# Optimization experiments

Measured on AMD Instinct MI355X. Metric: run time of the kernel, lower is better.

The kernel has to match this reference:

```python
import jax, jax.numpy as jnp
import numpy as np

N_NODES = 20000
NEG_SLOPE = 0.2  # PyG GATConv default leaky_relu slope


def segment_softmax(e, dst, num_segments):
    # e: [E, H] edge logits, softmax over edges sharing the same dst node
    m = jax.ops.segment_max(e, dst, num_segments=num_segments)
    ex = jnp.exp(e - m[dst])
    s = jax.ops.segment_sum(ex, dst, num_segments=num_segments)
    return ex / (s[dst] + 1e-16)


def gat_conv(x, src, dst, W, att_src, att_dst, bias, concat):
    # PyG GATConv (add_self_loops handled by caller). W: [Fin, H*C], att_*: [H, C]
    N = x.shape[0]
    H, C = att_src.shape
    h = (x @ W).reshape(N, H, C)
    a_src = jnp.einsum('nhc,hc->nh', h, att_src)  # [N, H]
    a_dst = jnp.einsum('nhc,hc->nh', h, att_dst)
    e = jax.nn.leaky_relu(a_src[src] + a_dst[dst], NEG_SLOPE)  # [E, H]
    alpha = segment_softmax(e, dst, N)
    msg = alpha[:, :, None] * h[src]  # [E, H, C]
    out = jax.ops.segment_sum(msg, dst, num_segments=N)  # [N, H, C]
    out = out.reshape(N, H * C) if concat else out.mean(axis=1)
    return out + bias


def add_self_loops(edge_index, num_nodes):
    loops = jnp.arange(num_nodes, dtype=edge_index.dtype)
    src = jnp.concatenate([edge_index[0], loops])
    dst = jnp.concatenate([edge_index[1], loops])
    return src, dst


def setup_inputs() -> dict:
    key = jax.random.key(0)
    ks = jax.random.split(key, 24)
    Fin, Hd, Hh, C2, Md = 1280, 256, 4, 128, 1024

    def w(k, shape, fan_in):
        return (jax.random.normal(k, shape, jnp.float32) * (1.0 / np.sqrt(fan_in))).astype(jnp.float32)

    return {
        'x': jax.random.normal(ks[0], (N_NODES, Fin), jnp.float32),
        'edge_index': jax.random.randint(ks[1], (2, 200000), 0, N_NODES, jnp.int32),
        'mutation_idx': 12345,
        'mutation_site_diff': jax.random.normal(ks[2], (1, Md), jnp.float32),
        # mutation_diff_processor: 1024 -> 128 -> 128
        'W_mut1': w(ks[3], (Md, 128), Md), 'b_mut1': jnp.zeros((128,), jnp.float32),
        'W_mut2': w(ks[4], (128, 128), 128), 'b_mut2': jnp.zeros((128,), jnp.float32),
        # GATConv1: Fin -> 256, 4 heads, concat
        'gat1_W': w(ks[5], (Fin, Hh * Hd), Fin),
        'gat1_as': w(ks[6], (Hh, Hd), Hd), 'gat1_ad': w(ks[7], (Hh, Hd), Hd),
        'gat1_b': jnp.zeros((Hh * Hd,), jnp.float32),
        # GATConv2: 1024 -> 128, 1 head
        'gat2_W': w(ks[8], (Hh * Hd, C2), Hh * Hd),
        'gat2_as': w(ks[9], (1, C2), C2), 'gat2_ad': w(ks[10], (1, C2), C2),
        'gat2_b': jnp.zeros((C2,), jnp.float32),
        # binding_predictor: 256 -> 128 -> 32 -> 1
        'W_p1': w(ks[11], (C2 + 128, 128), C2 + 128), 'b_p1': jnp.zeros((128,), jnp.float32),
        'W_p2': w(ks[12], (128, 32), 128), 'b_p2': jnp.zeros((32,), jnp.float32),
        'W_p3': w(ks[13], (32, 1), 32), 'b_p3': jnp.zeros((1,), jnp.float32),
    }


def reference(x, edge_index, mutation_idx, mutation_site_diff,
              W_mut1, b_mut1, W_mut2, b_mut2,
              gat1_W, gat1_as, gat1_ad, gat1_b,
              gat2_W, gat2_as, gat2_ad, gat2_b,
              W_p1, b_p1, W_p2, b_p2, W_p3, b_p3):
    src, dst = add_self_loops(edge_index, x.shape[0])
    # mutation diff MLP (dropout = identity at eval)
    pmd = jax.nn.relu(mutation_site_diff @ W_mut1 + b_mut1) @ W_mut2 + b_mut2
    h = jax.nn.relu(gat_conv(x, src, dst, gat1_W, gat1_as, gat1_ad, gat1_b, concat=True))
    h = jax.nn.relu(gat_conv(h, src, dst, gat2_W, gat2_as, gat2_ad, gat2_b, concat=False))
    feat = h[mutation_idx:mutation_idx + 1]  # [1, 128]
    z = jnp.concatenate([feat, pmd], axis=-1)
    z = jax.nn.relu(z @ W_p1 + b_p1)
    z = jax.nn.relu(z @ W_p2 + b_p2)
    return z @ W_p3 + b_p3
```

## Files before the change

### kernel.cpp

```cpp
#include <hip/hip_runtime.h>
#include <hip/hip_bf16.h>

#define NNODES 20000
#define NE_RAW 200000
#define NE_TOT 220000
#define MAX1   128
#define MAX2   512
#define MAXE1  4096
#define MAXE2  256
#define FIN    1280
#define FH     1024
#define HC     256
#define NHEAD  4
#define C2     128
#define CAPE   512
#define KCK    64
#define NKC    20
#define HH_GEMM_BLOCKS 320

__device__ __forceinline__ float lrelu(float x){ return x >= 0.f ? x : 0.2f * x; }

__global__ void k_init(int* cnt, int* slot1, int* slot2){
  int i = blockIdx.x * 256 + threadIdx.x;
  if (i < NNODES){ slot1[i] = -1; slot2[i] = -1; }
  if (i < 8) cnt[i] = 0;
}

__global__ void k_scan1(const int* __restrict__ ei, const int* __restrict__ mip,
                        int* cnt, int* slot1, int* S1, int* E2){
  int e = blockIdx.x * 256 + threadIdx.x;
  if (e >= NE_TOT) return;
  int mi = mip[0];
  int src, dst;
  if (e < NE_RAW){ src = ei[e]; dst = ei[NE_RAW + e]; }
  else { src = e - NE_RAW; dst = src; }
  if (dst != mi) return;
  int p = atomicAdd(&cnt[3], 1);
  if (p < MAXE2) E2[p] = src;
  if (atomicCAS(&slot1[src], -1, -9) == -1){
    int idx = atomicAdd(&cnt[0], 1);
    if (idx < MAX1){ S1[idx] = src; slot1[src] = idx; }
  }
}

__global__ void k_scan2(const int* __restrict__ ei, int* cnt,
                        const int* __restrict__ slot1, int* slot2,
                        int* S2, int* E1s, int* E1d){
  int e = blockIdx.x * 256 + threadIdx.x;
  if (e >= NE_TOT) return;
  int src, dst;
  if (e < NE_RAW){ src = ei[e]; dst = ei[NE_RAW + e]; }
  else { src = e - NE_RAW; dst = src; }
  if (slot1[dst] < 0) return;
  int p = atomicAdd(&cnt[2], 1);
  if (p < MAXE1){ E1s[p] = src; E1d[p] = dst; }
  if (atomicCAS(&slot2[src], -1, -9) == -1){
    int idx = atomicAdd(&cnt[1], 1);
    if (idx < MAX2){ S2[idx] = src; slot2[src] = idx; }
  }
}

__global__ __launch_bounds__(256) void k_hh(
    const float* __restrict__ x, const float* __restrict__ W1,
    const float* __restrict__ msd, const float* __restrict__ Wm1,
    const float* __restrict__ bm1,
    const int* __restrict__ cnt, const int* __restrict__ S2,
    float* __restrict__ hpart, float* __restrict__ r1){
  int t = threadIdx.x;
  if (blockIdx.x >= HH_GEMM_BLOCKS){
    __shared__ float red[256];
    int b   = blockIdx.x - HH_GEMM_BLOCKS;
    int col = b * 32 + (t & 31);
    int sl  = t >> 5;
    float s = 0.f;
    for (int k = sl * 128; k < sl * 128 + 128; ++k)
      s += msd[k] * Wm1[k * C2 + col];
    red[t] = s;
    __syncthreads();
    if (t < 32){
      float v = 0.f;
      #pragma unroll
      for (int q = 0; q < 8; ++q) v += red[q * 32 + t];
      v += bm1[col];
      r1[col] = v > 0.f ? v : 0.f;
    }
    return;
  }
  __shared__ float Wl[KCK][128];
  __shared__ float Xl[KCK][32];
  int bid = blockIdx.x;
  int rs = bid & 1, ct = (bid >> 1) & 7, kc = bid >> 4;
  int k0 = kc * KCK, c0 = ct * 128;
  int n2 = cnt[1]; if (n2 > MAX2) n2 = MAX2;
  for (int idx = t; idx < 2048; idx += 256){
    int r = idx >> 5, c4 = idx & 31;
    *(float4*)&Wl[r][c4 * 4] = *(const float4*)(W1 + (long)(k0 + r) * FH + c0 + c4 * 4);
  }
  int nRG = (n2 + 31) >> 5;
  int cth = t & 31, rth = t >> 5;
  for (int rg = rs; rg < nRG; rg += 2){
    int r0 = rg * 32;
    __syncthreads();
    for (int idx = t; idx < 512; idx += 256){
      int r = idx & 31, kq = idx >> 5;
      float4 v = make_float4(0.f, 0.f, 0.f, 0.f);
      if (r0 + r < n2)
        v = *(const float4*)(x + (long)S2[r0 + r] * FIN + k0 + kq * 4);
      Xl[kq * 4 + 0][r] = v.x;
      Xl[kq * 4 + 1][r] = v.y;
      Xl[kq * 4 + 2][r] = v.z;
      Xl[kq * 4 + 3][r] = v.w;
    }
    __syncthreads();
    float4 a0 = make_float4(0.f,0.f,0.f,0.f), a1 = a0, a2 = a0, a3 = a0;
    #pragma unroll 4
    for (int k = 0; k < KCK; ++k){
      float4 w  = *(const float4*)&Wl[k][cth * 4];
      float4 xv = *(const float4*)&Xl[k][rth * 4];
      a0.x += xv.x * w.x; a0.y += xv.x * w.y; a0.z += xv.x * w.z; a0.w += xv.x * w.w;
      a1.x += xv.y * w.x; a1.y += xv.y * w.y; a1.z += xv.y * w.z; a1.w += xv.y * w.w;
      a2.x += xv.z * w.x; a2.y += xv.z * w.y; a2.z += xv.z * w.z; a2.w += xv.z * w.w;
      a3.x += xv.w * w.x; a3.y += xv.w * w.y; a3.z += xv.w * w.z; a3.w += xv.w * w.w;
    }
    int rb = r0 + rth * 4;
    float* dp = hpart + ((long)kc * MAX2 + rb) * FH + c0 + cth * 4;
    if (rb + 0 < n2) *(float4*)(dp)            = a0;
    if (rb + 1 < n2) *(float4*)(dp + FH)       = a1;
    if (rb + 2 < n2) *(float4*)(dp + 2L * FH)  = a2;
    if (rb + 3 < n2) *(float4*)(dp + 3L * FH)  = a3;
  }
}

__global__ void k_ascal(const float* __restrict__ hpart,
                        const float* __restrict__ as1, const float* __restrict__ ad1,
                        const int* __restrict__ cnt,
                        float* __restrict__ hh,
                        float* __restrict__ asrc1, float* __restrict__ adst1){
  int t = threadIdx.x, head = t >> 6;
  int n2 = cnt[1]; if (n2 > MAX2) n2 = MAX2;
  float4 a = *(const float4*)(as1 + 4 * t);
  float4 d = *(const float4*)(ad1 + 4 * t);
  for (int i = blockIdx.x; i < n2; i += gridDim.x){
    float4 s = make_float4(0.f, 0.f, 0.f, 0.f);
    #pragma unroll
    for (int kc = 0; kc < NKC; ++kc){
      float4 v = *(const float4*)(hpart + ((long)kc * MAX2 + i) * FH + 4 * t);
      s.x += v.x; s.y += v.y; s.z += v.z; s.w += v.w;
    }
    *(float4*)(hh + (long)i * FH + 4 * t) = s;
    float ss = s.x * a.x + s.y * a.y + s.z * a.z + s.w * a.w;
    float sd = s.x * d.x + s.y * d.y + s.z * d.z + s.w * d.w;
    #pragma unroll
    for (int o = 32; o; o >>= 1){ ss += __shfl_xor(ss, o, 64); sd += __shfl_xor(sd, o, 64); }
    if ((t & 63) == 0){ asrc1[i * NHEAD + head] = ss; adst1[i * NHEAD + head] = sd; }
  }
}

__global__ __launch_bounds__(1024) void k_agg1(
    const float* __restrict__ hh,
    const float* __restrict__ asrc1, const float* __restrict__ adst1,
    const float* __restrict__ b1, const float* __restrict__ W2,
    const int* __restrict__ cnt, const int* __restrict__ S1,
    const int* __restrict__ slot2,
    const int* __restrict__ E1s, const int* __restrict__ E1d,
    float* __restrict__ gb){
  __shared__ int   lsrc[CAPE];
  __shared__ float ev[NHEAD][CAPE];
  __shared__ float h1row[FH];
  __shared__ float part[8][C2];
  __shared__ int   scnt;
  int t = threadIdx.x;
  int n1  = cnt[0]; if (n1  > MAX1)  n1  = MAX1;
  int nE1 = cnt[2]; if (nE1 > MAXE1) nE1 = MAXE1;
  for (int j = blockIdx.x; j < n1; j += gridDim.x){
    int s = S1[j];
    __syncthreads();
    if (t == 0) scnt = 0;
    __syncthreads();
    for (int e = t; e < nE1; e += 1024){
      if (E1d[e] == s){
        int q = atomicAdd(&scnt, 1);
        if (q < CAPE) lsrc[q] = slot2[E1s[e]];
      }
    }
    __syncthreads();
    int ce = scnt; if (ce > CAPE) ce = CAPE;
    if (t < 256){
      int w = t >> 6, lane = t & 63;
      float ad = adst1[slot2[s] * NHEAD + w];
      float m = -3.4e38f;
      for (int e = lane; e < ce; e += 64){
        float v = lrelu(asrc1[lsrc[e] * NHEAD + w] + ad);
        ev[w][e] = v;
        m = fmaxf(m, v);
      }
      #pragma unroll
      for (int o = 32; o; o >>= 1) m = fmaxf(m, __shfl_xor(m, o, 64));
      float ssum = 0.f;
      for (int e = lane; e < ce; e += 64){
        float a2 = expf(ev[w][e] - m);
        ev[w][e] = a2;
        ssum += a2;
      }
      #pragma unroll
      for (int o = 32; o; o >>= 1) ssum += __shfl_xor(ssum, o, 64);
      float inv = 1.f / (ssum + 1e-16f);
      for (int e = lane; e < ce; e += 64) ev[w][e] *= inv;
    }
    __syncthreads();
    if (t < 256){
      int hd = t >> 6;
      float4 accv = make_float4(0.f, 0.f, 0.f, 0.f);
      int e = 0;
      for (; e + 3 < ce; e += 4){
        float al0 = ev[hd][e],     al1 = ev[hd][e + 1];
        float al2 = ev[hd][e + 2], al3 = ev[hd][e + 3];
        float4 h0 = *(const float4*)(hh + (long)lsrc[e]     * FH + 4 * t);
        float4 h1 = *(const float4*)(hh + (long)lsrc[e + 1] * FH + 4 * t);
        float4 h2 = *(const float4*)(hh + (long)lsrc[e + 2] * FH + 4 * t);
        float4 h3 = *(const float4*)(hh + (long)lsrc[e + 3] * FH + 4 * t);
        accv.x += al0 * h0.x + al1 * h1.x + al2 * h2.x + al3 * h3.x;
        accv.y += al0 * h0.y + al1 * h1.y + al2 * h2.y + al3 * h3.y;
        accv.z += al0 * h0.z + al1 * h1.z + al2 * h2.z + al3 * h3.z;
        accv.w += al0 * h0.w + al1 * h1.w + al2 * h2.w + al3 * h3.w;
      }
      for (; e < ce; ++e){
        float al0 = ev[hd][e];
        float4 h0 = *(const float4*)(hh + (long)lsrc[e] * FH + 4 * t);
        accv.x += al0 * h0.x; accv.y += al0 * h0.y;
        accv.z += al0 * h0.z; accv.w += al0 * h0.w;
      }
      float4 bv = *(const float4*)(b1 + 4 * t);
      accv.x += bv.x; accv.y += bv.y; accv.z += bv.z; accv.w += bv.w;
      accv.x = accv.x > 0.f ? accv.x : 0.f;
      accv.y = accv.y > 0.f ? accv.y : 0.f;
      accv.z = accv.z > 0.f ? accv.z : 0.f;
      accv.w = accv.w > 0.f ? accv.w : 0.f;
      *(float4*)(h1row + 4 * t) = accv;
    }
    __syncthreads();
    {
      int col = t & 127, sl = t >> 7;
      const float* Wp = W2 + (long)(sl * 128) * C2 + col;
      const float* hp = h1row + sl * 128;
      float g = 0.f;
      #pragma unroll 16
      for (int k = 0; k < 128; ++k) g += hp[k] * Wp[(long)k * C2];
      part[sl][col] = g;
    }
    __syncthreads();
    if (t < C2){
      float s8 = 0.f;
      #pragma unroll
      for (int q = 0; q < 8; ++q) s8 += part[q][t];
      gb[j * C2 + t] = s8;
    }
  }
}

__global__ __launch_bounds__(512) void k_final(
    const int* __restrict__ mip, const int* __restrict__ cnt,
    const int* __restrict__ slot1, const int* __restrict__ E2,
    const float* __restrict__ gb,
    const float* __restrict__ as2, const float* __restrict__ ad2,
    const float* __restrict__ b2,
    const float* __restrict__ r1,
    const float* __restrict__ Wm2, const float* __restrict__ bm2,
    const float* __restrict__ Wp1, const float* __restrict__ bp1,
    const float* __restrict__ Wp2, const float* __restrict__ bp2,
    const float* __restrict__ Wp3, const float* __restrict__ bp3,
    float* __restrict__ out){
  __shared__ float al[MAXE2];
  __shared__ int   jl[MAXE2];
  __shared__ float feat[C2], r2s[C2], z1s[C2], z2s[32];
  __shared__ float p4[4][C2];
  __shared__ float p16[16][32];
  int t = threadIdx.x;
  int mi  = mip[0];
  int jmi = slot1[mi];
  int ne2 = cnt[3]; if (ne2 > MAXE2) ne2 = MAXE2;
  for (int k = t; k < ne2; k += 512) jl[k] = slot1[E2[k]];
  __syncthreads();
  int w = t >> 6, lane = t & 63;
  {
    int c = lane * 2;
    float v = gb[jmi * C2 + c] * ad2[c] + gb[jmi * C2 + c + 1] * ad2[c + 1];
    #pragma unroll
    for (int o = 32; o; o >>= 1) v += __shfl_xor(v, o, 64);
    float adv = v;
    for (int k = w; k < ne2; k += 8){
      int jj = jl[k];
      float u = gb[jj * C2 + c] * as2[c] + gb[jj * C2 + c + 1] * as2[c + 1];
      #pragma unroll
      for (int o = 32; o; o >>= 1) u += __shfl_xor(u, o, 64);
      if (lane == 0) al[k] = lrelu(u + adv);
    }
  }
  __syncthreads();
  if (t < 64){
    float m = -3.4e38f;
    for (int k = t; k < ne2; k += 64) m = fmaxf(m, al[k]);
    #pragma unroll
    for (int o = 32; o; o >>= 1) m = fmaxf(m, __shfl_xor(m, o, 64));
    float s = 0.f;
    for (int k = t; k < ne2; k += 64){
      float a2 = expf(al[k] - m);
      al[k] = a2;
      s += a2;
    }
    #pragma unroll
    for (int o = 32; o; o >>= 1) s += __shfl_xor(s, o, 64);
    float inv = 1.f / (s + 1e-16f);
    for (int k = t; k < ne2; k += 64) al[k] *= inv;
  }
  __syncthreads();
  int col = t & 127, sub = t >> 7;
  {
    float pr = 0.f;
    #pragma unroll 8
    for (int k = sub * 32; k < sub * 32 + 32; ++k) pr += r1[k] * Wm2[k * C2 + col];
    p4[sub][col] = pr;
    if (t < C2){
      float acc = 0.f;
      for (int k = 0; k < ne2; ++k) acc += al[k] * gb[jl[k] * C2 + t];
      float v = acc + b2[t];
      feat[t] = v > 0.f ? v : 0.f;
    }
  }
  __syncthreads();
  if (t < C2) r2s[t] = p4[0][t] + p4[1][t] + p4[2][t] + p4[3][t] + bm2[t];
  __syncthreads();
  {
    float acc = 0.f;
    #pragma unroll 8
    for (int k = sub * 64; k < sub * 64 + 64; ++k){
      float zv = (k < C2) ? feat[k] : r2s[k - C2];
      acc += zv * Wp1[k * C2 + col];
    }
    p4[sub][col] = acc;
  }
  __syncthreads();
  if (t < C2){
    float v = p4[0][t] + p4[1][t] + p4[2][t] + p4[3][t] + bp1[t];
    z1s[t] = v > 0.f ? v : 0.f;
  }
  __syncthreads();
  {
    int c2 = t & 31, sl = t >> 5;
    float acc = 0.f;
    #pragma unroll
    for (int k = sl * 8; k < sl * 8 + 8; ++k) acc += z1s[k] * Wp2[k * 32 + c2];
    p16[sl][c2] = acc;
  }
  __syncthreads();
  if (t < 32){
    float s = 0.f;
    #pragma unroll
    for (int q = 0; q < 16; ++q) s += p16[q][t];
    float v = s + bp2[t];
    z2s[t] = v > 0.f ? v : 0.f;
  }
  __syncthreads();
  if (t == 0){
    float acc = 0.f;
    for (int k = 0; k < 32; ++k) acc += z2s[k] * Wp3[k];
    out[0] = acc + bp3[0];
  }
}

extern "C" void kernel_launch(void* const* d_in, const int* in_sizes, int n_in,
                              void* d_out, int out_size, void* d_ws, size_t ws_size,
                              hipStream_t stream){
  const float* x   = (const float*)d_in[0];
  const int*   ei  = (const int*)d_in[1];
  const int*   mip = (const int*)d_in[2];
  const float* msd = (const float*)d_in[3];
  const float* Wm1 = (const float*)d_in[4];
  const float* bm1 = (const float*)d_in[5];
  const float* Wm2 = (const float*)d_in[6];
  const float* bm2 = (const float*)d_in[7];
  const float* W1  = (const float*)d_in[8];
  const float* as1 = (const float*)d_in[9];
  const float* ad1 = (const float*)d_in[10];
  const float* b1  = (const float*)d_in[11];
  const float* W2  = (const float*)d_in[12];
  const float* as2 = (const float*)d_in[13];
  const float* ad2 = (const float*)d_in[14];
  const float* b2  = (const float*)d_in[15];
  const float* Wp1 = (const float*)d_in[16];
  const float* bp1 = (const float*)d_in[17];
  const float* Wp2 = (const float*)d_in[18];
  const float* bp2 = (const float*)d_in[19];
  const float* Wp3 = (const float*)d_in[20];
  const float* bp3 = (const float*)d_in[21];
  float* out = (float*)d_out;

  char* q = (char*)d_ws;
  auto alloc = [&](size_t bytes) -> void* {
    void* r = (void*)q;
    q += (bytes + 255) & ~(size_t)255;
    return r;
  };
  int* cnt   = (int*)alloc(8 * 4);
  int* slot1 = (int*)alloc(NNODES * 4);
  int* slot2 = (int*)alloc(NNODES * 4);
  int* S1    = (int*)alloc(MAX1 * 4);
  int* S2    = (int*)alloc(MAX2 * 4);
  int* E1s   = (int*)alloc(MAXE1 * 4);
  int* E1d   = (int*)alloc(MAXE1 * 4);
  int* E2    = (int*)alloc(MAXE2 * 4);
  float* hpart = (float*)alloc((size_t)NKC * MAX2 * FH * 4);
  float* hh    = (float*)alloc((size_t)MAX2 * FH * 4);
  float* gb    = (float*)alloc(MAX1 * C2 * 4);
  float* asrc1 = (float*)alloc(MAX2 * NHEAD * 4);
  float* adst1 = (float*)alloc(MAX2 * NHEAD * 4);
  float* r1    = (float*)alloc(C2 * 4);

  k_init <<<(NNODES + 255) / 256, 256, 0, stream>>>(cnt, slot1, slot2);
  k_scan1<<<(NE_TOT + 255) / 256, 256, 0, stream>>>(ei, mip, cnt, slot1, S1, E2);
  k_scan2<<<(NE_TOT + 255) / 256, 256, 0, stream>>>(ei, cnt, slot1, slot2, S2, E1s, E1d);
  k_hh   <<<HH_GEMM_BLOCKS + 4, 256, 0, stream>>>(x, W1, msd, Wm1, bm1, cnt, S2, hpart, r1);
  k_ascal<<<128, 256, 0, stream>>>(hpart, as1, ad1, cnt, hh, asrc1, adst1);
  k_agg1 <<<32, 1024, 0, stream>>>(hh, asrc1, adst1, b1, W2, cnt, S1, slot2, E1s, E1d, gb);
  k_final<<<1, 512, 0, stream>>>(mip, cnt, slot1, E2, gb, as2, ad2, b2, r1,
                                 Wm2, bm2, Wp1, bp1, Wp2, bp2, Wp3, bp3, out);
}
```

Measured before the change: 67.42 us.

## Replace split-K partial buffer with atomic accumulation and fuse attention scalars into agg1

The split-K GEMM now accumulates its partial products directly into hh with float atomicAdd, which removes the 20-slice partial buffer and the separate k_ascal reduction kernel. hh is zeroed inside k_init. The per-node attention logits (asrc, adst) are now computed inside k_agg1 from hh by wavefront dot products, instead of being read from precomputed arrays. This cuts one kernel launch and a large partial-sum write/read, but adds atomic contention from 20 K-chunks per output element, non-deterministic summation order, and redundant a_src recomputation per edge.

```diff
diff --git a/kernel.cpp b/kernel.cpp
--- a/kernel.cpp
+++ b/kernel.cpp
@@ -16,14 +16,19 @@
 #define CAPE   512
 #define KCK    64
 #define NKC    20
+#define NRS    2
+#define HH_PMD_BLOCKS 4
 #define HH_GEMM_BLOCKS 320
+#define INIT_BLOCKS 79
 
 __device__ __forceinline__ float lrelu(float x){ return x >= 0.f ? x : 0.2f * x; }
 
-__global__ void k_init(int* cnt, int* slot1, int* slot2){
+__global__ void k_init(int* cnt, int* slot1, int* slot2, float4* hhz){
   int i = blockIdx.x * 256 + threadIdx.x;
   if (i < NNODES){ slot1[i] = -1; slot2[i] = -1; }
   if (i < 8) cnt[i] = 0;
+  float4 z = make_float4(0.f, 0.f, 0.f, 0.f);
+  for (int v = i; v < MAX2 * FH / 4; v += INIT_BLOCKS * 256) hhz[v] = z;
 }
 
 __global__ void k_scan1(const int* __restrict__ ei, const int* __restrict__ mip,
@@ -65,11 +70,11 @@
     const float* __restrict__ msd, const float* __restrict__ Wm1,
     const float* __restrict__ bm1,
     const int* __restrict__ cnt, const int* __restrict__ S2,
-    float* __restrict__ hpart, float* __restrict__ r1){
+    float* __restrict__ hh, float* __restrict__ r1){
   int t = threadIdx.x;
-  if (blockIdx.x >= HH_GEMM_BLOCKS){
+  if (blockIdx.x < HH_PMD_BLOCKS){
     __shared__ float red[256];
-    int b   = blockIdx.x - HH_GEMM_BLOCKS;
+    int b   = blockIdx.x;
     int col = b * 32 + (t & 31);
     int sl  = t >> 5;
     float s = 0.f;
@@ -88,7 +93,7 @@
   }
   __shared__ float Wl[KCK][128];
   __shared__ float Xl[KCK][32];
-  int bid = blockIdx.x;
+  int bid = blockIdx.x - HH_PMD_BLOCKS;
   int rs = bid & 1, ct = (bid >> 1) & 7, kc = bid >> 4;
   int k0 = kc * KCK, c0 = ct * 128;
   int n2 = cnt[1]; if (n2 > MAX2) n2 = MAX2;
@@ -98,7 +103,7 @@
   }
   int nRG = (n2 + 31) >> 5;
   int cth = t & 31, rth = t >> 5;
-  for (int rg = rs; rg < nRG; rg += 2){
+  for (int rg = rs; rg < nRG; rg += NRS){
     int r0 = rg * 32;
     __syncthreads();
     for (int idx = t; idx < 512; idx += 256){
@@ -123,42 +128,32 @@
       a3.x += xv.w * w.x; a3.y += xv.w * w.y; a3.z += xv.w * w.z; a3.w += xv.w * w.w;
     }
     int rb = r0 + rth * 4;
-    float* dp = hpart + ((long)kc * MAX2 + rb) * FH + c0 + cth * 4;
-    if (rb + 0 < n2) *(float4*)(dp)            = a0;
-    if (rb + 1 < n2) *(float4*)(dp + FH)       = a1;
-    if (rb + 2 < n2) *(float4*)(dp + 2L * FH)  = a2;
-    if (rb + 3 < n2) *(float4*)(dp + 3L * FH)  = a3;
-  }
-}
-
-__global__ void k_ascal(const float* __restrict__ hpart,
-                        const float* __restrict__ as1, const float* __restrict__ ad1,
-                        const int* __restrict__ cnt,
-                        float* __restrict__ hh,
-                        float* __restrict__ asrc1, float* __restrict__ adst1){
-  int t = threadIdx.x, head = t >> 6;
-  int n2 = cnt[1]; if (n2 > MAX2) n2 = MAX2;
-  float4 a = *(const float4*)(as1 + 4 * t);
-  float4 d = *(const float4*)(ad1 + 4 * t);
-  for (int i = blockIdx.x; i < n2; i += gridDim.x){
-    float4 s = make_float4(0.f, 0.f, 0.f, 0.f);
-    #pragma unroll
-    for (int kc = 0; kc < NKC; ++kc){
-      float4 v = *(const float4*)(hpart + ((long)kc * MAX2 + i) * FH + 4 * t);
-      s.x += v.x; s.y += v.y; s.z += v.z; s.w += v.w;
-    }
-    *(float4*)(hh + (long)i * FH + 4 * t) = s;
-    float ss = s.x * a.x + s.y * a.y + s.z * a.z + s.w * a.w;
-    float sd = s.x * d.x + s.y * d.y + s.z * d.z + s.w * d.w;
-    #pragma unroll
-    for (int o = 32; o; o >>= 1){ ss += __shfl_xor(ss, o, 64); sd += __shfl_xor(sd, o, 64); }
-    if ((t & 63) == 0){ asrc1[i * NHEAD + head] = ss; adst1[i * NHEAD + head] = sd; }
+    float* dp = hh + (long)rb * FH + c0 + cth * 4;
+    if (rb + 0 < n2){
+      atomicAdd(dp + 0, a0.x); atomicAdd(dp + 1, a0.y);
+      atomicAdd(dp + 2, a0.z); atomicAdd(dp + 3, a0.w);
+    }
+    if (rb + 1 < n2){
+      float* d1 = dp + FH;
+      atomicAdd(d1 + 0, a1.x); atomicAdd(d1 + 1, a1.y);
+      atomicAdd(d1 + 2, a1.z); atomicAdd(d1 + 3, a1.w);
+    }
+    if (rb + 2 < n2){
+      float* d2 = dp + 2L * FH;
+      atomicAdd(d2 + 0, a2.x); atomicAdd(d2 + 1, a2.y);
+      atomicAdd(d2 + 2, a2.z); atomicAdd(d2 + 3, a2.w);
+    }
+    if (rb + 3 < n2){
+      float* d3 = dp + 3L * FH;
+      atomicAdd(d3 + 0, a3.x); atomicAdd(d3 + 1, a3.y);
+      atomicAdd(d3 + 2, a3.z); atomicAdd(d3 + 3, a3.w);
+    }
   }
 }
 
 __global__ __launch_bounds__(1024) void k_agg1(
     const float* __restrict__ hh,
-    const float* __restrict__ asrc1, const float* __restrict__ adst1,
+    const float* __restrict__ as1, const float* __restrict__ ad1,
     const float* __restrict__ b1, const float* __restrict__ W2,
     const int* __restrict__ cnt, const int* __restrict__ S1,
     const int* __restrict__ slot2,
@@ -166,6 +161,7 @@
     float* __restrict__ gb){
   __shared__ int   lsrc[CAPE];
   __shared__ float ev[NHEAD][CAPE];
+  __shared__ float adml[NHEAD];
   __shared__ float h1row[FH];
   __shared__ float part[8][C2];
   __shared__ int   scnt;
@@ -185,12 +181,44 @@
     }
     __syncthreads();
     int ce = scnt; if (ce > CAPE) ce = CAPE;
+    int w = t >> 6, lane = t & 63;
     if (t < 256){
-      int w = t >> 6, lane = t & 63;
-      float ad = adst1[slot2[s] * NHEAD + w];
+      float4 a = *(const float4*)(as1 + 4 * t);
+      float4 d = *(const float4*)(ad1 + 4 * t);
+      {
+        float4 hv = *(const float4*)(hh + (long)slot2[s] * FH + 4 * t);
+        float sd = hv.x * d.x + hv.y * d.y + hv.z * d.z + hv.w * d.w;
+        #pragma unroll
+        for (int o = 32; o; o >>= 1) sd += __shfl_xor(sd, o, 64);
+        if (lane == 0) adml[w] = sd;
+      }
+      int e = 0;
+      for (; e + 1 < ce; e += 2){
+        float4 h0 = *(const float4*)(hh + (long)lsrc[e]     * FH + 4 * t);
+        float4 h1 = *(const float4*)(hh + (long)lsrc[e + 1] * FH + 4 * t);
+        float s0 = h0.x * a.x + h0.y * a.y + h0.z * a.z + h0.w * a.w;
+        float s1 = h1.x * a.x + h1.y * a.y + h1.z * a.z + h1.w * a.w;
+        #pragma unroll
+        for (int o = 32; o; o >>= 1){
+          s0 += __shfl_xor(s0, o, 64);
+          s1 += __shfl_xor(s1, o, 64);
+        }
+        if (lane == 0){ ev[w][e] = s0; ev[w][e + 1] = s1; }
+      }
+      if (e < ce){
+        float4 h0 = *(const float4*)(hh + (long)lsrc[e] * FH + 4 * t);
+        float s0 = h0.x * a.x + h0.y * a.y + h0.z * a.z + h0.w * a.w;
+        #pragma unroll
+        for (int o = 32; o; o >>= 1) s0 += __shfl_xor(s0, o, 64);
+        if (lane == 0) ev[w][e] = s0;
+      }
+    }
+    __syncthreads();
+    if (t < 256){
+      float adv = adml[w];
       float m = -3.4e38f;
       for (int e = lane; e < ce; e += 64){
-        float v = lrelu(asrc1[lsrc[e] * NHEAD + w] + ad);
+        float v = lrelu(ev[w][e] + adv);
         ev[w][e] = v;
         m = fmaxf(m, v);
       }
@@ -409,19 +437,15 @@
   int* E1s   = (int*)alloc(MAXE1 * 4);
   int* E1d   = (int*)alloc(MAXE1 * 4);
   int* E2    = (int*)alloc(MAXE2 * 4);
-  float* hpart = (float*)alloc((size_t)NKC * MAX2 * FH * 4);
-  float* hh    = (float*)alloc((size_t)MAX2 * FH * 4);
-  float* gb    = (float*)alloc(MAX1 * C2 * 4);
-  float* asrc1 = (float*)alloc(MAX2 * NHEAD * 4);
-  float* adst1 = (float*)alloc(MAX2 * NHEAD * 4);
-  float* r1    = (float*)alloc(C2 * 4);
-
-  k_init <<<(NNODES + 255) / 256, 256, 0, stream>>>(cnt, slot1, slot2);
+  float* hh  = (float*)alloc((size_t)MAX2 * FH * 4);
+  float* gb  = (float*)alloc(MAX1 * C2 * 4);
+  float* r1  = (float*)alloc(C2 * 4);
+
+  k_init <<<INIT_BLOCKS, 256, 0, stream>>>(cnt, slot1, slot2, (float4*)hh);
   k_scan1<<<(NE_TOT + 255) / 256, 256, 0, stream>>>(ei, mip, cnt, slot1, S1, E2);
   k_scan2<<<(NE_TOT + 255) / 256, 256, 0, stream>>>(ei, cnt, slot1, slot2, S2, E1s, E1d);
-  k_hh   <<<HH_GEMM_BLOCKS + 4, 256, 0, stream>>>(x, W1, msd, Wm1, bm1, cnt, S2, hpart, r1);
-  k_ascal<<<128, 256, 0, stream>>>(hpart, as1, ad1, cnt, hh, asrc1, adst1);
-  k_agg1 <<<32, 1024, 0, stream>>>(hh, asrc1, adst1, b1, W2, cnt, S1, slot2, E1s, E1d, gb);
+  k_hh   <<<HH_PMD_BLOCKS + HH_GEMM_BLOCKS, 256, 0, stream>>>(x, W1, msd, Wm1, bm1, cnt, S2, hh, r1);
+  k_agg1 <<<32, 1024, 0, stream>>>(hh, as1, ad1, b1, W2, cnt, S1, slot2, E1s, E1d, gb);
   k_final<<<1, 512, 0, stream>>>(mip, cnt, slot1, E2, gb, as2, ad2, b2, r1,
                                  Wm2, bm2, Wp1, bp1, Wp2, bp2, Wp3, bp3, out);
 }
```

Result: slower. 73.69 us (+9.3%).

## Reorder layer-1 GAT math to aggregate raw features before projecting by W1

Applied to the files above, without the earlier changes.

Folds the attention vectors into W1 (w_att = W1·att) so attention logits come straight from x, then aggregates raw x rows per head with softmax weights and only afterwards multiplies the per-head aggregates by W1. This removes the projection of every 2-hop neighbor (up to 512 rows) and the hh/slot2 bookkeeping, shrinking the GEMM to the 1-hop set of at most 128 rows times 4 heads. Scan kernels now read four edges per thread with int4 loads. The cost is a per-call W1·att reduction over all of W1 and per-edge dot products over x rows of length 1280.

```diff
diff --git a/kernel.cpp b/kernel.cpp
--- a/kernel.cpp
+++ b/kernel.cpp
@@ -5,72 +5,39 @@
 #define NE_RAW 200000
 #define NE_TOT 220000
 #define MAX1   128
-#define MAX2   512
 #define MAXE1  4096
 #define MAXE2  256
 #define FIN    1280
 #define FH     1024
-#define HC     256
 #define NHEAD  4
 #define C2     128
 #define CAPE   512
 #define KCK    64
 #define NKC    20
-#define HH_GEMM_BLOCKS 320
+#define INIT_B 79
+#define A_B    160
+#define PMD_B  4
+#define D_B    160
 
 __device__ __forceinline__ float lrelu(float x){ return x >= 0.f ? x : 0.2f * x; }
 
-__global__ void k_init(int* cnt, int* slot1, int* slot2){
-  int i = blockIdx.x * 256 + threadIdx.x;
-  if (i < NNODES){ slot1[i] = -1; slot2[i] = -1; }
-  if (i < 8) cnt[i] = 0;
-}
-
-__global__ void k_scan1(const int* __restrict__ ei, const int* __restrict__ mip,
-                        int* cnt, int* slot1, int* S1, int* E2){
-  int e = blockIdx.x * 256 + threadIdx.x;
-  if (e >= NE_TOT) return;
-  int mi = mip[0];
-  int src, dst;
-  if (e < NE_RAW){ src = ei[e]; dst = ei[NE_RAW + e]; }
-  else { src = e - NE_RAW; dst = src; }
-  if (dst != mi) return;
-  int p = atomicAdd(&cnt[3], 1);
-  if (p < MAXE2) E2[p] = src;
-  if (atomicCAS(&slot1[src], -1, -9) == -1){
-    int idx = atomicAdd(&cnt[0], 1);
-    if (idx < MAX1){ S1[idx] = src; slot1[src] = idx; }
-  }
-}
-
-__global__ void k_scan2(const int* __restrict__ ei, int* cnt,
-                        const int* __restrict__ slot1, int* slot2,
-                        int* S2, int* E1s, int* E1d){
-  int e = blockIdx.x * 256 + threadIdx.x;
-  if (e >= NE_TOT) return;
-  int src, dst;
-  if (e < NE_RAW){ src = ei[e]; dst = ei[NE_RAW + e]; }
-  else { src = e - NE_RAW; dst = src; }
-  if (slot1[dst] < 0) return;
-  int p = atomicAdd(&cnt[2], 1);
-  if (p < MAXE1){ E1s[p] = src; E1d[p] = dst; }
-  if (atomicCAS(&slot2[src], -1, -9) == -1){
-    int idx = atomicAdd(&cnt[1], 1);
-    if (idx < MAX2){ S2[idx] = src; slot2[src] = idx; }
-  }
-}
-
-__global__ __launch_bounds__(256) void k_hh(
-    const float* __restrict__ x, const float* __restrict__ W1,
+__global__ __launch_bounds__(256) void k_init_a(
+    const float* __restrict__ W1, const float* __restrict__ as1,
+    const float* __restrict__ ad1,
     const float* __restrict__ msd, const float* __restrict__ Wm1,
     const float* __restrict__ bm1,
-    const int* __restrict__ cnt, const int* __restrict__ S2,
-    float* __restrict__ hpart, float* __restrict__ r1){
-  int t = threadIdx.x;
-  if (blockIdx.x >= HH_GEMM_BLOCKS){
+    int* cnt, int* slot1, float* __restrict__ w_att, float* __restrict__ r1){
+  int t = threadIdx.x, b = blockIdx.x;
+  if (b < INIT_B){
+    int i = b * 256 + t;
+    if (i < NNODES) slot1[i] = -1;
+    if (i < 8) cnt[i] = 0;
+    return;
+  }
+  if (b >= INIT_B + A_B){
     __shared__ float red[256];
-    int b   = blockIdx.x - HH_GEMM_BLOCKS;
-    int col = b * 32 + (t & 31);
+    int pb  = b - INIT_B - A_B;
+    int col = pb * 32 + (t & 31);
     int sl  = t >> 5;
     float s = 0.f;
     for (int k = sl * 128; k < sl * 128 + 128; ++k)
@@ -86,90 +53,99 @@
     }
     return;
   }
-  __shared__ float Wl[KCK][128];
-  __shared__ float Xl[KCK][32];
-  int bid = blockIdx.x;
-  int rs = bid & 1, ct = (bid >> 1) & 7, kc = bid >> 4;
-  int k0 = kc * KCK, c0 = ct * 128;
-  int n2 = cnt[1]; if (n2 > MAX2) n2 = MAX2;
-  for (int idx = t; idx < 2048; idx += 256){
-    int r = idx >> 5, c4 = idx & 31;
-    *(float4*)&Wl[r][c4 * 4] = *(const float4*)(W1 + (long)(k0 + r) * FH + c0 + c4 * 4);
-  }
-  int nRG = (n2 + 31) >> 5;
-  int cth = t & 31, rth = t >> 5;
-  for (int rg = rs; rg < nRG; rg += 2){
-    int r0 = rg * 32;
-    __syncthreads();
-    for (int idx = t; idx < 512; idx += 256){
-      int r = idx & 31, kq = idx >> 5;
-      float4 v = make_float4(0.f, 0.f, 0.f, 0.f);
-      if (r0 + r < n2)
-        v = *(const float4*)(x + (long)S2[r0 + r] * FIN + k0 + kq * 4);
-      Xl[kq * 4 + 0][r] = v.x;
-      Xl[kq * 4 + 1][r] = v.y;
-      Xl[kq * 4 + 2][r] = v.z;
-      Xl[kq * 4 + 3][r] = v.w;
-    }
-    __syncthreads();
-    float4 a0 = make_float4(0.f,0.f,0.f,0.f), a1 = a0, a2 = a0, a3 = a0;
-    #pragma unroll 4
-    for (int k = 0; k < KCK; ++k){
-      float4 w  = *(const float4*)&Wl[k][cth * 4];
-      float4 xv = *(const float4*)&Xl[k][rth * 4];
-      a0.x += xv.x * w.x; a0.y += xv.x * w.y; a0.z += xv.x * w.z; a0.w += xv.x * w.w;
-      a1.x += xv.y * w.x; a1.y += xv.y * w.y; a1.z += xv.y * w.z; a1.w += xv.y * w.w;
-      a2.x += xv.z * w.x; a2.y += xv.z * w.y; a2.z += xv.z * w.z; a2.w += xv.z * w.w;
-      a3.x += xv.w * w.x; a3.y += xv.w * w.y; a3.z += xv.w * w.z; a3.w += xv.w * w.w;
-    }
-    int rb = r0 + rth * 4;
-    float* dp = hpart + ((long)kc * MAX2 + rb) * FH + c0 + cth * 4;
-    if (rb + 0 < n2) *(float4*)(dp)            = a0;
-    if (rb + 1 < n2) *(float4*)(dp + FH)       = a1;
-    if (rb + 2 < n2) *(float4*)(dp + 2L * FH)  = a2;
-    if (rb + 3 < n2) *(float4*)(dp + 3L * FH)  = a3;
-  }
-}
-
-__global__ void k_ascal(const float* __restrict__ hpart,
-                        const float* __restrict__ as1, const float* __restrict__ ad1,
-                        const int* __restrict__ cnt,
-                        float* __restrict__ hh,
-                        float* __restrict__ asrc1, float* __restrict__ adst1){
-  int t = threadIdx.x, head = t >> 6;
-  int n2 = cnt[1]; if (n2 > MAX2) n2 = MAX2;
-  float4 a = *(const float4*)(as1 + 4 * t);
-  float4 d = *(const float4*)(ad1 + 4 * t);
-  for (int i = blockIdx.x; i < n2; i += gridDim.x){
-    float4 s = make_float4(0.f, 0.f, 0.f, 0.f);
-    #pragma unroll
-    for (int kc = 0; kc < NKC; ++kc){
-      float4 v = *(const float4*)(hpart + ((long)kc * MAX2 + i) * FH + 4 * t);
-      s.x += v.x; s.y += v.y; s.z += v.z; s.w += v.w;
-    }
-    *(float4*)(hh + (long)i * FH + 4 * t) = s;
-    float ss = s.x * a.x + s.y * a.y + s.z * a.z + s.w * a.w;
-    float sd = s.x * d.x + s.y * d.y + s.z * d.z + s.w * d.w;
-    #pragma unroll
-    for (int o = 32; o; o >>= 1){ ss += __shfl_xor(ss, o, 64); sd += __shfl_xor(sd, o, 64); }
-    if ((t & 63) == 0){ asrc1[i * NHEAD + head] = ss; adst1[i * NHEAD + head] = sd; }
-  }
-}
-
-__global__ __launch_bounds__(1024) void k_agg1(
-    const float* __restrict__ hh,
-    const float* __restrict__ asrc1, const float* __restrict__ adst1,
-    const float* __restrict__ b1, const float* __restrict__ W2,
+  __shared__ float red[4][8];
+  int kbase = (b - INIT_B) * 8;
+  int w = t >> 6, lane = t & 63;
+  float av0 = as1[t], av1 = as1[t + 256], av2 = as1[t + 512], av3 = as1[t + 768];
+  float dv0 = ad1[t], dv1 = ad1[t + 256], dv2 = ad1[t + 512], dv3 = ad1[t + 768];
+  for (int rr = 0; rr < 8; ++rr){
+    int k = kbase + rr;
+    const float* Wr = W1 + (long)k * FH;
+    float w0 = Wr[t], w1 = Wr[t + 256], w2 = Wr[t + 512], w3 = Wr[t + 768];
+    float v[8] = { w0*av0, w1*av1, w2*av2, w3*av3, w0*dv0, w1*dv1, w2*dv2, w3*dv3 };
+    #pragma unroll
+    for (int q = 0; q < 8; ++q){
+      float s = v[q];
+      #pragma unroll
+      for (int o = 32; o; o >>= 1) s += __shfl_xor(s, o, 64);
+      if (lane == 0) red[w][q] = s;
+      __syncthreads();
+      if (t == 0) w_att[k * 8 + q] = red[0][q] + red[1][q] + red[2][q] + red[3][q];
+      __syncthreads();
+    }
+  }
+}
+
+__global__ void k_scan1(const int* __restrict__ ei, const int* __restrict__ mip,
+                        int* cnt, int* slot1, int* S1, int* E2){
+  int e0 = (blockIdx.x * 256 + threadIdx.x) * 4;
+  if (e0 >= NE_TOT) return;
+  int mi = mip[0];
+  int s[4], d[4], n = 0;
+  if (e0 + 3 < NE_RAW){
+    int4 s4 = *(const int4*)(ei + e0);
+    int4 d4 = *(const int4*)(ei + NE_RAW + e0);
+    s[0]=s4.x; s[1]=s4.y; s[2]=s4.z; s[3]=s4.w;
+    d[0]=d4.x; d[1]=d4.y; d[2]=d4.z; d[3]=d4.w;
+    n = 4;
+  } else {
+    for (int q = 0; q < 4; ++q){
+      int e = e0 + q;
+      if (e >= NE_TOT) break;
+      if (e < NE_RAW){ s[n] = ei[e]; d[n] = ei[NE_RAW + e]; }
+      else { s[n] = e - NE_RAW; d[n] = s[n]; }
+      ++n;
+    }
+  }
+  for (int q = 0; q < n; ++q){
+    if (d[q] != mi) continue;
+    int p = atomicAdd(&cnt[3], 1);
+    if (p < MAXE2) E2[p] = s[q];
+    if (atomicCAS(&slot1[s[q]], -1, -9) == -1){
+      int idx = atomicAdd(&cnt[0], 1);
+      if (idx < MAX1){ S1[idx] = s[q]; slot1[s[q]] = idx; }
+    }
+  }
+}
+
+__global__ void k_scan2(const int* __restrict__ ei, int* cnt,
+                        const int* __restrict__ slot1, int* E1s, int* E1d){
+  int e0 = (blockIdx.x * 256 + threadIdx.x) * 4;
+  if (e0 >= NE_TOT) return;
+  int s[4], d[4], n = 0;
+  if (e0 + 3 < NE_RAW){
+    int4 s4 = *(const int4*)(ei + e0);
+    int4 d4 = *(const int4*)(ei + NE_RAW + e0);
+    s[0]=s4.x; s[1]=s4.y; s[2]=s4.z; s[3]=s4.w;
+    d[0]=d4.x; d[1]=d4.y; d[2]=d4.z; d[3]=d4.w;
+    n = 4;
+  } else {
+    for (int q = 0; q < 4; ++q){
+      int e = e0 + q;
+      if (e >= NE_TOT) break;
+      if (e < NE_RAW){ s[n] = ei[e]; d[n] = ei[NE_RAW + e]; }
+      else { s[n] = e - NE_RAW; d[n] = s[n]; }
+      ++n;
+    }
+  }
+  for (int q = 0; q < n; ++q){
+    if (slot1[d[q]] < 0) continue;
+    int p = atomicAdd(&cnt[2], 1);
+    if (p < MAXE1){ E1s[p] = s[q]; E1d[p] = d[q]; }
+  }
+}
+
+__global__ __launch_bounds__(256) void k_bc(
+    const float* __restrict__ x, const float* __restrict__ w_att,
     const int* __restrict__ cnt, const int* __restrict__ S1,
-    const int* __restrict__ slot2,
     const int* __restrict__ E1s, const int* __restrict__ E1d,
-    float* __restrict__ gb){
+    float* __restrict__ X1){
   __shared__ int   lsrc[CAPE];
   __shared__ float ev[NHEAD][CAPE];
-  __shared__ float h1row[FH];
-  __shared__ float part[8][C2];
+  __shared__ float adml[NHEAD];
+  __shared__ float redl[4][4];
   __shared__ int   scnt;
-  int t = threadIdx.x;
+  int t = threadIdx.x, w = t >> 6, lane = t & 63;
   int n1  = cnt[0]; if (n1  > MAX1)  n1  = MAX1;
   int nE1 = cnt[2]; if (nE1 > MAXE1) nE1 = MAXE1;
   for (int j = blockIdx.x; j < n1; j += gridDim.x){
@@ -177,20 +153,59 @@
     __syncthreads();
     if (t == 0) scnt = 0;
     __syncthreads();
-    for (int e = t; e < nE1; e += 1024){
+    for (int e = t; e < nE1; e += 256){
       if (E1d[e] == s){
         int q = atomicAdd(&scnt, 1);
-        if (q < CAPE) lsrc[q] = slot2[E1s[e]];
+        if (q < CAPE) lsrc[q] = E1s[e];
       }
     }
     __syncthreads();
     int ce = scnt; if (ce > CAPE) ce = CAPE;
-    if (t < 256){
-      int w = t >> 6, lane = t & 63;
-      float ad = adst1[slot2[s] * NHEAD + w];
+    {
+      const float* xs = x + (long)s * FIN;
+      float a0=0.f, a1=0.f, a2=0.f, a3=0.f;
+      #pragma unroll
+      for (int i = 0; i < 5; ++i){
+        int k = t + 256 * i;
+        float xv = xs[k];
+        float4 wd = *(const float4*)(w_att + k * 8 + 4);
+        a0 += xv * wd.x; a1 += xv * wd.y; a2 += xv * wd.z; a3 += xv * wd.w;
+      }
+      float v[4] = { a0, a1, a2, a3 };
+      #pragma unroll
+      for (int q = 0; q < 4; ++q){
+        float sv = v[q];
+        #pragma unroll
+        for (int o = 32; o; o >>= 1) sv += __shfl_xor(sv, o, 64);
+        if (lane == 0) redl[w][q] = sv;
+      }
+      __syncthreads();
+      if (t < 4) adml[t] = redl[0][t] + redl[1][t] + redl[2][t] + redl[3][t];
+      __syncthreads();
+    }
+    for (int e = w; e < ce; e += 4){
+      const float* xe = x + (long)lsrc[e] * FIN;
+      float b0=0.f, b1v=0.f, b2v=0.f, b3v=0.f;
+      #pragma unroll 4
+      for (int i = 0; i < 20; ++i){
+        int k = lane + 64 * i;
+        float xv = xe[k];
+        float4 ws = *(const float4*)(w_att + k * 8);
+        b0 += xv * ws.x; b1v += xv * ws.y; b2v += xv * ws.z; b3v += xv * ws.w;
+      }
+      #pragma unroll
+      for (int o = 32; o; o >>= 1){
+        b0  += __shfl_xor(b0, o, 64);  b1v += __shfl_xor(b1v, o, 64);
+        b2v += __shfl_xor(b2v, o, 64); b3v += __shfl_xor(b3v, o, 64);
+      }
+      if (lane == 0){ ev[0][e]=b0; ev[1][e]=b1v; ev[2][e]=b2v; ev[3][e]=b3v; }
+    }
+    __syncthreads();
+    {
+      float ad = adml[w];
       float m = -3.4e38f;
       for (int e = lane; e < ce; e += 64){
-        float v = lrelu(asrc1[lsrc[e] * NHEAD + w] + ad);
+        float v = lrelu(ev[w][e] + ad);
         ev[w][e] = v;
         m = fmaxf(m, v);
       }
@@ -208,35 +223,93 @@
       for (int e = lane; e < ce; e += 64) ev[w][e] *= inv;
     }
     __syncthreads();
+    {
+      float acc[20];
+      #pragma unroll
+      for (int i = 0; i < 20; ++i) acc[i] = 0.f;
+      for (int e = 0; e < ce; ++e){
+        float al = ev[w][e];
+        const float* xe = x + (long)lsrc[e] * FIN;
+        #pragma unroll
+        for (int i = 0; i < 20; ++i) acc[i] += al * xe[lane + 64 * i];
+      }
+      float* X1p = X1 + ((long)j * NHEAD + w) * FIN;
+      #pragma unroll
+      for (int i = 0; i < 20; ++i) X1p[lane + 64 * i] = acc[i];
+    }
+    __syncthreads();
+  }
+}
+
+__global__ __launch_bounds__(256) void k_d(
+    const float* __restrict__ X1, const float* __restrict__ W1,
+    const int* __restrict__ cnt, float* __restrict__ hpart){
+  __shared__ float Wl[KCK][128];
+  __shared__ float Xl[KCK][16];
+  int t = threadIdx.x, bid = blockIdx.x;
+  int ct = bid & 7, kc = bid >> 3;
+  int head = ct >> 1;
+  int k0 = kc * KCK, c0 = ct * 128;
+  int n1 = cnt[0]; if (n1 > MAX1) n1 = MAX1;
+  for (int idx = t; idx < 2048; idx += 256){
+    int r = idx >> 5, c4 = idx & 31;
+    *(float4*)&Wl[r][c4 * 4] = *(const float4*)(W1 + (long)(k0 + r) * FH + c0 + c4 * 4);
+  }
+  int nRG = (n1 + 15) >> 4;
+  int cth = t & 31, rth = t >> 5;
+  for (int rg = 0; rg < nRG; ++rg){
+    int r0 = rg * 16;
+    __syncthreads();
+    {
+      int r = t & 15, kq = t >> 4;
+      float4 v = make_float4(0.f, 0.f, 0.f, 0.f);
+      if (r0 + r < n1)
+        v = *(const float4*)(X1 + ((long)(r0 + r) * NHEAD + head) * FIN + k0 + kq * 4);
+      Xl[kq * 4 + 0][r] = v.x;
+      Xl[kq * 4 + 1][r] = v.y;
+      Xl[kq * 4 + 2][r] = v.z;
+      Xl[kq * 4 + 3][r] = v.w;
+    }
+    __syncthreads();
+    float4 A0 = make_float4(0.f,0.f,0.f,0.f), A1 = A0;
+    #pragma unroll 4
+    for (int k = 0; k < KCK; ++k){
+      float4 wv = *(const float4*)&Wl[k][cth * 4];
+      float x0 = Xl[k][rth * 2], x1 = Xl[k][rth * 2 + 1];
+      A0.x += x0 * wv.x; A0.y += x0 * wv.y; A0.z += x0 * wv.z; A0.w += x0 * wv.w;
+      A1.x += x1 * wv.x; A1.y += x1 * wv.y; A1.z += x1 * wv.z; A1.w += x1 * wv.w;
+    }
+    int rb = r0 + rth * 2;
+    float* dp = hpart + ((long)kc * MAX1 + rb) * FH + c0 + cth * 4;
+    if (rb < n1)     *(float4*)(dp)      = A0;
+    if (rb + 1 < n1) *(float4*)(dp + FH) = A1;
+  }
+}
+
+__global__ __launch_bounds__(1024) void k_e(
+    const float* __restrict__ hpart, const float* __restrict__ b1,
+    const float* __restrict__ W2, const int* __restrict__ cnt,
+    float* __restrict__ gb){
+  __shared__ float h1row[FH];
+  __shared__ float part[8][C2];
+  int t = threadIdx.x;
+  int n1 = cnt[0]; if (n1 > MAX1) n1 = MAX1;
+  for (int j = blockIdx.x; j < n1; j += gridDim.x){
+    __syncthreads();
     if (t < 256){
-      int hd = t >> 6;
-      float4 accv = make_float4(0.f, 0.f, 0.f, 0.f);
-      int e = 0;
-      for (; e + 3 < ce; e += 4){
-        float al0 = ev[hd][e],     al1 = ev[hd][e + 1];
-        float al2 = ev[hd][e + 2], al3 = ev[hd][e + 3];
-        float4 h0 = *(const float4*)(hh + (long)lsrc[e]     * FH + 4 * t);
-        float4 h1 = *(const float4*)(hh + (long)lsrc[e + 1] * FH + 4 * t);
-        float4 h2 = *(const float4*)(hh + (long)lsrc[e + 2] * FH + 4 * t);
-        float4 h3 = *(const float4*)(hh + (long)lsrc[e + 3] * FH + 4 * t);
-        accv.x += al0 * h0.x + al1 * h1.x + al2 * h2.x + al3 * h3.x;
-        accv.y += al0 * h0.y + al1 * h1.y + al2 * h2.y + al3 * h3.y;
-        accv.z += al0 * h0.z + al1 * h1.z + al2 * h2.z + al3 * h3.z;
-        accv.w += al0 * h0.w + al1 * h1.w + al2 * h2.w + al3 * h3.w;
-      }
-      for (; e < ce; ++e){
-        float al0 = ev[hd][e];
-        float4 h0 = *(const float4*)(hh + (long)lsrc[e] * FH + 4 * t);
-        accv.x += al0 * h0.x; accv.y += al0 * h0.y;
-        accv.z += al0 * h0.z; accv.w += al0 * h0.w;
+      float4 s = make_float4(0.f, 0.f, 0.f, 0.f);
+      #pragma unroll
+      for (int kc = 0; kc < NKC; ++kc){
+        float4 v = *(const float4*)(hpart + ((long)kc * MAX1 + j) * FH + 4 * t);
+        s.x += v.x; s.y += v.y; s.z += v.z; s.w += v.w;
       }
       float4 bv = *(const float4*)(b1 + 4 * t);
-      accv.x += bv.x; accv.y += bv.y; accv.z += bv.z; accv.w += bv.w;
-      accv.x = accv.x > 0.f ? accv.x : 0.f;
-      accv.y = accv.y > 0.f ? accv.y : 0.f;
-      accv.z = accv.z > 0.f ? accv.z : 0.f;
-      accv.w = accv.w > 0.f ? accv.w : 0.f;
-      *(float4*)(h1row + 4 * t) = accv;
+      s.x += bv.x; s.y += bv.y; s.z += bv.z; s.w += bv.w;
+      s.x = s.x > 0.f ? s.x : 0.f;
+      s.y = s.y > 0.f ? s.y : 0.f;
+      s.z = s.z > 0.f ? s.z : 0.f;
+      s.w = s.w > 0.f ? s.w : 0.f;
+      *(float4*)(h1row + 4 * t) = s;
     }
     __syncthreads();
     {
@@ -403,25 +476,23 @@
   };
   int* cnt   = (int*)alloc(8 * 4);
   int* slot1 = (int*)alloc(NNODES * 4);
-  int* slot2 = (int*)alloc(NNODES * 4);
   int* S1    = (int*)alloc(MAX1 * 4);
-  int* S2    = (int*)alloc(MAX2 * 4);
   int* E1s   = (int*)alloc(MAXE1 * 4);
   int* E1d   = (int*)alloc(MAXE1 * 4);
   int* E2    = (int*)alloc(MAXE2 * 4);
-  float* hpart = (float*)alloc((size_t)NKC * MAX2 * FH * 4);
-  float* hh    = (float*)alloc((size_t)MAX2 * FH * 4);
+  float* w_att = (float*)alloc((size_t)FIN * 8 * 4);
+  float* X1    = (float*)alloc((size_t)MAX1 * NHEAD * FIN * 4);
+  float* hpart = (float*)alloc((size_t)NKC * MAX1 * FH * 4);
   float* gb    = (float*)alloc(MAX1 * C2 * 4);
-  float* asrc1 = (float*)alloc(MAX2 * NHEAD * 4);
-  float* adst1 = (float*)alloc(MAX2 * NHEAD * 4);
   float* r1    = (float*)alloc(C2 * 4);
 
-  k_init <<<(NNODES + 255) / 256, 256, 0, stream>>>(cnt, slot1, slot2);
-  k_scan1<<<(NE_TOT + 255) / 256, 256, 0, stream>>>(ei, mip, cnt, slot1, S1, E2);
-  k_scan2<<<(NE_TOT + 255) / 256, 256, 0, stream>>>(ei, cnt, slot1, slot2, S2, E1s, E1d);
-  k_hh   <<<HH_GEMM_BLOCKS + 4, 256, 0, stream>>>(x, W1, msd, Wm1, bm1, cnt, S2, hpart, r1);
-  k_ascal<<<128, 256, 0, stream>>>(hpart, as1, ad1, cnt, hh, asrc1, adst1);
-  k_agg1 <<<32, 1024, 0, stream>>>(hh, asrc1, adst1, b1, W2, cnt, S1, slot2, E1s, E1d, gb);
+  k_init_a<<<INIT_B + A_B + PMD_B, 256, 0, stream>>>(W1, as1, ad1, msd, Wm1, bm1,
+                                                     cnt, slot1, w_att, r1);
+  k_scan1<<<(NE_TOT + 1023) / 1024, 256, 0, stream>>>(ei, mip, cnt, slot1, S1, E2);
+  k_scan2<<<(NE_TOT + 1023) / 1024, 256, 0, stream>>>(ei, cnt, slot1, E1s, E1d);
+  k_bc   <<<32, 256, 0, stream>>>(x, w_att, cnt, S1, E1s, E1d, X1);
+  k_d    <<<D_B, 256, 0, stream>>>(X1, W1, cnt, hpart);
+  k_e    <<<16, 1024, 0, stream>>>(hpart, b1, W2, cnt, gb);
   k_final<<<1, 512, 0, stream>>>(mip, cnt, slot1, E2, gb, as2, ad2, b2, r1,
                                  Wm2, bm2, Wp1, bp1, Wp2, bp2, Wp3, bp3, out);
 }
```

Result: slower. 68.97 us (+2.3%).
